# Performance work log

Measured on AMD Instinct MI355X. Metric: run time of the kernel, lower is better.

## Reference

```python
import jax, jax.numpy as jnp
import numpy as np

HIDDEN = 128
N_NODES = 50000
N_EDGES = 600000


def setup_inputs() -> dict:
    key = jax.random.key(0)
    k_h, k_s, k_d, k_w1, k_b1, k_w2, k_b2 = jax.random.split(key, 7)
    h = jax.random.normal(k_h, (N_NODES, HIDDEN), dtype=jnp.float32)
    src = jax.random.randint(k_s, (N_EDGES,), 0, N_NODES, dtype=jnp.int64)
    dst = jax.random.randint(k_d, (N_EDGES,), 0, N_NODES, dtype=jnp.int64)
    # link_predictor params: Linear(2H -> H), Linear(H -> 1)
    lim1 = 1.0 / np.sqrt(2 * HIDDEN)
    W1 = jax.random.uniform(k_w1, (2 * HIDDEN, HIDDEN), dtype=jnp.float32, minval=-lim1, maxval=lim1)
    b1 = jax.random.uniform(k_b1, (HIDDEN,), dtype=jnp.float32, minval=-lim1, maxval=lim1)
    lim2 = 1.0 / np.sqrt(HIDDEN)
    W2 = jax.random.uniform(k_w2, (HIDDEN, 1), dtype=jnp.float32, minval=-lim2, maxval=lim2)
    b2 = jax.random.uniform(k_b2, (1,), dtype=jnp.float32, minval=-lim2, maxval=lim2)
    return {"h": h, "W1": W1, "b1": b1, "W2": W2, "b2": b2, "src": src, "dst": dst}


def reference(h, W1, b1, W2, b2, src, dst):
    # per-edge gather of source/destination node features, concat -> [E, 2H]
    h_cat = jnp.concatenate([h[src], h[dst]], axis=1)
    hid = jax.nn.relu(h_cat @ W1 + b1)           # [E, H]
    score = jax.nn.sigmoid(hid @ W2 + b2)        # [E, 1]
    return score.squeeze(-1)                     # [E]
```

## Files before the change

kernel.cpp:

```cpp
#include <hip/hip_runtime.h>
#include <hip/hip_bf16.h>


#define HID    128
#define NNODE  50000
#define NEDGE  600000
#define NGRP   ((NNODE + 31) / 32)
#define NUNIT  ((NGRP + 1) / 2)
#define K1BLK  320
#define K2BLK  1536

typedef __attribute__((ext_vector_type(8)))  __bf16 bf16x8;
typedef __attribute__((ext_vector_type(16))) float  f32x16;

static __device__ __forceinline__ unsigned int pack2bf(float a, float b) {
    unsigned int ua = __float_as_uint(a);
    unsigned int ub = __float_as_uint(b);
    ua = (ua + 0x7FFFu + ((ua >> 16) & 1u)) >> 16;
    ub = (ub + 0x7FFFu + ((ub >> 16) & 1u)) >> 16;
    return (ub << 16) | (ua & 0xFFFFu);
}

__global__ __launch_bounds__(256, 2) void node_gemm_kernel(
    const float* __restrict__ h, const float* __restrict__ W1,
    unsigned short* __restrict__ uvs)
{
    __shared__ unsigned char smem[65536];
    const int t = threadIdx.x, lane = t & 63, wv = t >> 6;
    const int l31 = lane & 31, l5 = lane >> 5;

    for (int task = t; task < 4096; task += 256) {
        int n = task & 255, slot = task >> 8;
        const float* wp = (n < 128) ? (W1 + (slot * 8) * HID + n)
                                    : (W1 + (128 + slot * 8) * HID + (n - 128));
        bf16x8 v;
#pragma unroll
        for (int j = 0; j < 8; ++j) v[j] = (__bf16)wp[j * HID];
        *(bf16x8*)(smem + n * 256 + ((slot * 16) ^ ((n & 15) << 4))) = v;
    }
    __syncthreads();

    const int nof0 = (wv & 1) * 128;

    for (int unit = blockIdx.x; unit < NUNIT; unit += K1BLK) {
        const int group = unit * 2 + (wv >> 1);
        if (group >= NGRP) continue;

        const int node  = group * 32 + l31;
        const int nodec = node < NNODE ? node : NNODE - 1;
        const float* hp = h + (size_t)nodec * HID + l5 * 8;

        f32x16 acc[4];
#pragma unroll
        for (int ct = 0; ct < 4; ++ct)
#pragma unroll
            for (int r = 0; r < 16; ++r) acc[ct][r] = 0.0f;

#pragma unroll
        for (int ks = 0; ks < 8; ++ks) {
            float4 f0 = *(const float4*)(hp + ks * 16);
            float4 f1 = *(const float4*)(hp + ks * 16 + 4);
            bf16x8 af;
            af[0] = (__bf16)f0.x; af[1] = (__bf16)f0.y;
            af[2] = (__bf16)f0.z; af[3] = (__bf16)f0.w;
            af[4] = (__bf16)f1.x; af[5] = (__bf16)f1.y;
            af[6] = (__bf16)f1.z; af[7] = (__bf16)f1.w;
            const int koff = ks * 32 + l5 * 16;
#pragma unroll
            for (int ct = 0; ct < 4; ++ct) {
                const int n = nof0 + ct * 32 + l31;
                bf16x8 bfg = *(const bf16x8*)(smem + n * 256 +
                                              (koff ^ ((n & 15) << 4)));
                acc[ct] = __builtin_amdgcn_mfma_f32_32x32x16_bf16(af, bfg,
                                                                  acc[ct], 0, 0, 0);
            }
        }

#pragma unroll
        for (int ct = 0; ct < 4; ++ct) {
#pragma unroll
            for (int r = 0; r < 16; ++r) {
                float mine = acc[ct][r];
                float partner = __shfl_xor(mine, 1);
                if (!(l31 & 1)) {
                    const int rr = (r & 3) + 8 * (r >> 2) + 4 * l5;
                    const int nd = group * 32 + rr;
                    if (nd < NNODE) {
                        const int n = nof0 + ct * 32 + l31;
                        *(unsigned int*)(uvs + (size_t)nd * 256 + n) =
                            pack2bf(mine, partner);
                    }
                }
            }
        }
    }
}

__global__ __launch_bounds__(256, 6) void edge_score_kernel(
    const unsigned short* __restrict__ uvs, const float* __restrict__ b1,
    const float* __restrict__ W2, const float* __restrict__ b2,
    const int* __restrict__ src, const int* __restrict__ dst,
    float* __restrict__ out)
{
    const int t = threadIdx.x, lane = t & 63, wv = t >> 6;
    const int c = lane & 15;
    const int g = lane >> 4;

    bool idx64;
    {
        unsigned long long m =
            __ballot((src[2 * lane + 1] == 0) && (dst[2 * lane + 1] == 0));
        idx64 = (m == ~0ULL);
    }

    float b1f[8], w2f[8];
#pragma unroll
    for (int j = 0; j < 8; ++j) {
        b1f[j] = b1[c * 8 + j];
        w2f[j] = W2[c * 8 + j];
    }
    const float b2s = b2[0];

    const int gw = blockIdx.x * 4 + wv;
    const int NQ = NEDGE / 4;
    for (int q = gw; q < NQ; q += K2BLK * 4) {
        const int e  = q * 4 + g;
        const int ns = idx64 ? src[2 * e] : src[e];
        const int nd = idx64 ? dst[2 * e] : dst[e];
        const uint4 qu = *(const uint4*)(uvs + (size_t)ns * 256 + c * 8);
        const uint4 qv = *(const uint4*)(uvs + (size_t)nd * 256 + 128 + c * 8);

        float p = 0.0f;
#pragma unroll
        for (int j = 0; j < 4; ++j) {
            const unsigned int uw = j == 0 ? qu.x : j == 1 ? qu.y : j == 2 ? qu.z : qu.w;
            const unsigned int vw = j == 0 ? qv.x : j == 1 ? qv.y : j == 2 ? qv.z : qv.w;
            float slo = __uint_as_float(uw << 16) + __uint_as_float(vw << 16)
                        + b1f[2 * j];
            float shi = __uint_as_float(uw & 0xFFFF0000u)
                        + __uint_as_float(vw & 0xFFFF0000u) + b1f[2 * j + 1];
            slo = slo > 0.0f ? slo : 0.0f;
            shi = shi > 0.0f ? shi : 0.0f;
            p = fmaf(slo, w2f[2 * j], p);
            p = fmaf(shi, w2f[2 * j + 1], p);
        }
        p += __shfl_xor(p, 1);
        p += __shfl_xor(p, 2);
        p += __shfl_xor(p, 4);
        p += __shfl_xor(p, 8);

        if (c == 0)
            out[e] = 1.0f / (1.0f + __expf(-(p + b2s)));
    }
}

extern "C" void kernel_launch(void* const* d_in, const int* in_sizes, int n_in,
                              void* d_out, int out_size, void* d_ws, size_t ws_size,
                              hipStream_t stream) {
    const float* h  = (const float*)d_in[0];
    const float* W1 = (const float*)d_in[1];
    const float* b1 = (const float*)d_in[2];
    const float* W2 = (const float*)d_in[3];
    const float* b2 = (const float*)d_in[4];
    const int* src  = (const int*)d_in[5];
    const int* dst  = (const int*)d_in[6];
    (void)in_sizes; (void)n_in; (void)out_size; (void)ws_size;

    node_gemm_kernel<<<K1BLK, 256, 0, stream>>>(h, W1, (unsigned short*)d_ws);
    edge_score_kernel<<<K2BLK, 256, 0, stream>>>(
        (const unsigned short*)d_ws, b1, W2, b2, src, dst, (float*)d_out);
}
```

Baseline: 76.17 us.

## Fold b1 into node GEMM, one group per block, 2-edge ILP in edge kernel

The node GEMM kernel now folds b1 into the u half of the projection, so the edge kernel no longer adds the bias. The node kernel launches one block per unit pair instead of a persistent grid. That adds many blocks, each re-staging W1 into shared memory. The edge kernel processes two edge quads per iteration to put more gathers in flight, raises its occupancy hint, and uses more blocks. Folding b1 before bf16 rounding changes the rounding slightly.

```diff
diff --git a/kernel.cpp b/kernel.cpp
--- a/kernel.cpp
+++ b/kernel.cpp
@@ -6,9 +6,8 @@
 #define NNODE  50000
 #define NEDGE  600000
 #define NGRP   ((NNODE + 31) / 32)
-#define NUNIT  ((NGRP + 1) / 2)
-#define K1BLK  320
-#define K2BLK  1536
+#define K1BLK  ((NGRP + 1) / 2)
+#define K2BLK  2048
 
 typedef __attribute__((ext_vector_type(8)))  __bf16 bf16x8;
 typedef __attribute__((ext_vector_type(16))) float  f32x16;
@@ -23,7 +22,7 @@
 
 __global__ __launch_bounds__(256, 2) void node_gemm_kernel(
     const float* __restrict__ h, const float* __restrict__ W1,
-    unsigned short* __restrict__ uvs)
+    const float* __restrict__ b1, unsigned short* __restrict__ uvs)
 {
     __shared__ unsigned char smem[65536];
     const int t = threadIdx.x, lane = t & 63, wv = t >> 6;
@@ -40,64 +39,66 @@
     }
     __syncthreads();
 
+    const int group = blockIdx.x * 2 + (wv >> 1);
+    if (group >= NGRP) return;
     const int nof0 = (wv & 1) * 128;
 
-    for (int unit = blockIdx.x; unit < NUNIT; unit += K1BLK) {
-        const int group = unit * 2 + (wv >> 1);
-        if (group >= NGRP) continue;
+    const float baddf = (nof0 == 0) ? 1.0f : 0.0f;
+    float b1v[4];
+#pragma unroll
+    for (int ct = 0; ct < 4; ++ct) b1v[ct] = baddf * b1[ct * 32 + l31];
 
-        const int node  = group * 32 + l31;
-        const int nodec = node < NNODE ? node : NNODE - 1;
-        const float* hp = h + (size_t)nodec * HID + l5 * 8;
+    const int node  = group * 32 + l31;
+    const int nodec = node < NNODE ? node : NNODE - 1;
+    const float* hp = h + (size_t)nodec * HID + l5 * 8;
 
-        f32x16 acc[4];
+    f32x16 acc[4];
 #pragma unroll
-        for (int ct = 0; ct < 4; ++ct)
+    for (int ct = 0; ct < 4; ++ct)
 #pragma unroll
-            for (int r = 0; r < 16; ++r) acc[ct][r] = 0.0f;
+        for (int r = 0; r < 16; ++r) acc[ct][r] = 0.0f;
 
 #pragma unroll
-        for (int ks = 0; ks < 8; ++ks) {
-            float4 f0 = *(const float4*)(hp + ks * 16);
-            float4 f1 = *(const float4*)(hp + ks * 16 + 4);
-            bf16x8 af;
-            af[0] = (__bf16)f0.x; af[1] = (__bf16)f0.y;
-            af[2] = (__bf16)f0.z; af[3] = (__bf16)f0.w;
-            af[4] = (__bf16)f1.x; af[5] = (__bf16)f1.y;
-            af[6] = (__bf16)f1.z; af[7] = (__bf16)f1.w;
-            const int koff = ks * 32 + l5 * 16;
+    for (int ks = 0; ks < 8; ++ks) {
+        float4 f0 = *(const float4*)(hp + ks * 16);
+        float4 f1 = *(const float4*)(hp + ks * 16 + 4);
+        bf16x8 af;
+        af[0] = (__bf16)f0.x; af[1] = (__bf16)f0.y;
+        af[2] = (__bf16)f0.z; af[3] = (__bf16)f0.w;
+        af[4] = (__bf16)f1.x; af[5] = (__bf16)f1.y;
+        af[6] = (__bf16)f1.z; af[7] = (__bf16)f1.w;
+        const int koff = ks * 32 + l5 * 16;
 #pragma unroll
-            for (int ct = 0; ct < 4; ++ct) {
-                const int n = nof0 + ct * 32 + l31;
-                bf16x8 bfg = *(const bf16x8*)(smem + n * 256 +
-                                              (koff ^ ((n & 15) << 4)));
-                acc[ct] = __builtin_amdgcn_mfma_f32_32x32x16_bf16(af, bfg,
-                                                                  acc[ct], 0, 0, 0);
-            }
+        for (int ct = 0; ct < 4; ++ct) {
+            const int n = nof0 + ct * 32 + l31;
+            bf16x8 bfg = *(const bf16x8*)(smem + n * 256 +
+                                          (koff ^ ((n & 15) << 4)));
+            acc[ct] = __builtin_amdgcn_mfma_f32_32x32x16_bf16(af, bfg,
+                                                              acc[ct], 0, 0, 0);
         }
+    }
 
 #pragma unroll
-        for (int ct = 0; ct < 4; ++ct) {
+    for (int ct = 0; ct < 4; ++ct) {
 #pragma unroll
-            for (int r = 0; r < 16; ++r) {
-                float mine = acc[ct][r];
-                float partner = __shfl_xor(mine, 1);
-                if (!(l31 & 1)) {
-                    const int rr = (r & 3) + 8 * (r >> 2) + 4 * l5;
-                    const int nd = group * 32 + rr;
-                    if (nd < NNODE) {
-                        const int n = nof0 + ct * 32 + l31;
-                        *(unsigned int*)(uvs + (size_t)nd * 256 + n) =
-                            pack2bf(mine, partner);
-                    }
+        for (int r = 0; r < 16; ++r) {
+            float mine = acc[ct][r] + b1v[ct];
+            float partner = __shfl_xor(mine, 1);
+            if (!(l31 & 1)) {
+                const int rr = (r & 3) + 8 * (r >> 2) + 4 * l5;
+                const int nd = group * 32 + rr;
+                if (nd < NNODE) {
+                    const int n = nof0 + ct * 32 + l31;
+                    *(unsigned int*)(uvs + (size_t)nd * 256 + n) =
+                        pack2bf(mine, partner);
                 }
             }
         }
     }
 }
 
-__global__ __launch_bounds__(256, 6) void edge_score_kernel(
-    const unsigned short* __restrict__ uvs, const float* __restrict__ b1,
+__global__ __launch_bounds__(256, 8) void edge_score_kernel(
+    const unsigned short* __restrict__ uvs,
     const float* __restrict__ W2, const float* __restrict__ b2,
     const int* __restrict__ src, const int* __restrict__ dst,
     float* __restrict__ out)
@@ -113,44 +114,61 @@
         idx64 = (m == ~0ULL);
     }
 
-    float b1f[8], w2f[8];
+    float w2f[8];
 #pragma unroll
-    for (int j = 0; j < 8; ++j) {
-        b1f[j] = b1[c * 8 + j];
-        w2f[j] = W2[c * 8 + j];
-    }
+    for (int j = 0; j < 8; ++j) w2f[j] = W2[c * 8 + j];
     const float b2s = b2[0];
 
     const int gw = blockIdx.x * 4 + wv;
+    const int NW = K2BLK * 4;
     const int NQ = NEDGE / 4;
-    for (int q = gw; q < NQ; q += K2BLK * 4) {
-        const int e  = q * 4 + g;
-        const int ns = idx64 ? src[2 * e] : src[e];
-        const int nd = idx64 ? dst[2 * e] : dst[e];
-        const uint4 qu = *(const uint4*)(uvs + (size_t)ns * 256 + c * 8);
-        const uint4 qv = *(const uint4*)(uvs + (size_t)nd * 256 + 128 + c * 8);
 
-        float p = 0.0f;
+    for (int q0 = gw; q0 < NQ; q0 += 2 * NW) {
+        const int q1  = q0 + NW;
+        const int q1c = q1 < NQ ? q1 : NQ - 1;
+        const int e0  = q0 * 4 + g;
+        const int e1  = q1c * 4 + g;
+
+        const int ns0 = idx64 ? src[2 * e0] : src[e0];
+        const int nd0 = idx64 ? dst[2 * e0] : dst[e0];
+        const int ns1 = idx64 ? src[2 * e1] : src[e1];
+        const int nd1 = idx64 ? dst[2 * e1] : dst[e1];
+
+        const uint4 qu0 = *(const uint4*)(uvs + (size_t)ns0 * 256 + c * 8);
+        const uint4 qv0 = *(const uint4*)(uvs + (size_t)nd0 * 256 + 128 + c * 8);
+        const uint4 qu1 = *(const uint4*)(uvs + (size_t)ns1 * 256 + c * 8);
+        const uint4 qv1 = *(const uint4*)(uvs + (size_t)nd1 * 256 + 128 + c * 8);
+
 #pragma unroll
-        for (int j = 0; j < 4; ++j) {
-            const unsigned int uw = j == 0 ? qu.x : j == 1 ? qu.y : j == 2 ? qu.z : qu.w;
-            const unsigned int vw = j == 0 ? qv.x : j == 1 ? qv.y : j == 2 ? qv.z : qv.w;
-            float slo = __uint_as_float(uw << 16) + __uint_as_float(vw << 16)
-                        + b1f[2 * j];
-            float shi = __uint_as_float(uw & 0xFFFF0000u)
-                        + __uint_as_float(vw & 0xFFFF0000u) + b1f[2 * j + 1];
-            slo = slo > 0.0f ? slo : 0.0f;
-            shi = shi > 0.0f ? shi : 0.0f;
-            p = fmaf(slo, w2f[2 * j], p);
-            p = fmaf(shi, w2f[2 * j + 1], p);
+        for (int half = 0; half < 2; ++half) {
+            const uint4 qu = half ? qu1 : qu0;
+            const uint4 qv = half ? qv1 : qv0;
+            float p = 0.0f;
+#pragma unroll
+            for (int j = 0; j < 4; ++j) {
+                const unsigned int uw = j == 0 ? qu.x : j == 1 ? qu.y
+                                      : j == 2 ? qu.z : qu.w;
+                const unsigned int vw = j == 0 ? qv.x : j == 1 ? qv.y
+                                      : j == 2 ? qv.z : qv.w;
+                float slo = __uint_as_float(uw << 16)
+                          + __uint_as_float(vw << 16);
+                float shi = __uint_as_float(uw & 0xFFFF0000u)
+                          + __uint_as_float(vw & 0xFFFF0000u);
+                slo = slo > 0.0f ? slo : 0.0f;
+                shi = shi > 0.0f ? shi : 0.0f;
+                p = fmaf(slo, w2f[2 * j], p);
+                p = fmaf(shi, w2f[2 * j + 1], p);
+            }
+            p += __shfl_xor(p, 1);
+            p += __shfl_xor(p, 2);
+            p += __shfl_xor(p, 4);
+            p += __shfl_xor(p, 8);
+
+            if (c == 0 && (half == 0 || q1 < NQ)) {
+                const int e = half ? e1 : e0;
+                out[e] = 1.0f / (1.0f + __expf(-(p + b2s)));
+            }
         }
-        p += __shfl_xor(p, 1);
-        p += __shfl_xor(p, 2);
-        p += __shfl_xor(p, 4);
-        p += __shfl_xor(p, 8);
-
-        if (c == 0)
-            out[e] = 1.0f / (1.0f + __expf(-(p + b2s)));
     }
 }
 
@@ -166,7 +184,8 @@
     const int* dst  = (const int*)d_in[6];
     (void)in_sizes; (void)n_in; (void)out_size; (void)ws_size;
 
-    node_gemm_kernel<<<K1BLK, 256, 0, stream>>>(h, W1, (unsigned short*)d_ws);
+    node_gemm_kernel<<<K1BLK, 256, 0, stream>>>(h, W1, b1,
+                                                (unsigned short*)d_ws);
     edge_score_kernel<<<K2BLK, 256, 0, stream>>>(
-        (const unsigned short*)d_ws, b1, W2, b2, src, dst, (float*)d_out);
+        (const unsigned short*)d_ws, W2, b2, src, dst, (float*)d_out);
 }
```

Result: no change. 75.88 us (-0.4%).
